# Performance work log

Measured on AMD Instinct MI355X. Metric: run time of the kernel, lower is better.

Reference implementation:

```python
import jax, jax.numpy as jnp
import numpy as np

N, E, R, D, P = 40000, 640000, 500, 128, 3

def setup_inputs() -> dict:
    key = jax.random.key(0)
    ks = jax.random.split(key, 14)
    return {
        "h": jax.random.normal(ks[0], (N, D), jnp.float32),
        "pos_enc": jax.random.normal(ks[1], (N, P), jnp.float32),
        "norm": jax.random.uniform(ks[2], (N, 1), jnp.float32),
        "emb_rel": jax.random.normal(ks[3], (R, D), jnp.float32),
        "W_hp": jax.random.normal(ks[4], (D + P, D), jnp.float32) / np.sqrt(D + P),
        "b_hp": jax.random.normal(ks[5], (D,), jnp.float32) * 0.01,
        "weight_neighbor": jax.random.normal(ks[6], (D, D), jnp.float32) / np.sqrt(D),
        "loop_weight": jax.random.normal(ks[7], (D, D), jnp.float32) / np.sqrt(D),
        "evolve_loop_weight": jax.random.normal(ks[8], (D, D), jnp.float32) / np.sqrt(D),
        "loop_weight_p": jax.random.normal(ks[9], (P, P), jnp.float32),
        "evolve_loop_weight_p": jax.random.normal(ks[10], (P, P), jnp.float32),
        "edge_src": jax.random.randint(ks[11], (E,), 0, N),
        "edge_dst": jax.random.randint(ks[12], (E,), 0, N),
        "edge_type": jax.random.randint(ks[13], (E,), 0, R),
    }

def reference(h, pos_enc, norm, emb_rel, W_hp, b_hp, weight_neighbor,
              loop_weight, evolve_loop_weight, loop_weight_p, evolve_loop_weight_p,
              edge_src, edge_dst, edge_type):
    n = h.shape[0]
    # self-loop: nodes with in-degree > 0 use loop_weight, else evolve_loop_weight
    in_deg = jax.ops.segment_sum(jnp.ones_like(edge_dst, dtype=h.dtype), edge_dst, num_segments=n)
    has_in = (in_deg > 0)[:, None]
    loop_msg = jnp.where(has_in, h @ loop_weight, h @ evolve_loop_weight)
    loop_msg_p = jnp.where(has_in, pos_enc @ loop_weight_p, pos_enc @ evolve_loop_weight_p)
    # per-edge message: embedding_hp(cat(h_src, pos_src)) + rel_emb[type], then weight_neighbor
    src_feat = jnp.concatenate([h[edge_src], pos_enc[edge_src]], axis=1)  # [E, D+P]
    e_h = src_feat @ W_hp + b_hp                                          # [E, D]
    msg = (e_h + emb_rel[edge_type]) @ weight_neighbor                    # [E, D]
    # scatter-sum to destination nodes, then norm scaling (apply_func)
    agg = jax.ops.segment_sum(msg, edge_dst, num_segments=n) * norm       # [N, D]
    node_repr = jax.nn.relu(agg + loop_msg)
    pos_out = jax.nn.relu(pos_enc + loop_msg_p)
    return node_repr, pos_out
```

## Files before the change

### kernel.cpp

```cpp
#include <hip/hip_runtime.h>


#define BS 1536
#define CAP2 48
#define CH 8192

typedef __bf16 bf16x8 __attribute__((ext_vector_type(8)));
typedef float f32x4 __attribute__((ext_vector_type(4)));
typedef unsigned short u16x4 __attribute__((ext_vector_type(4)));

__device__ inline unsigned short f2bf(float f) {
    unsigned u = __float_as_uint(f);
    u += 0x7fffu + ((u >> 16) & 1u);
    return (unsigned short)(u >> 16);
}
__device__ inline float bflo(unsigned u) { return __uint_as_float(u << 16); }
__device__ inline float bfhi(unsigned u) { return __uint_as_float(u & 0xffff0000u); }

__global__ __launch_bounds__(256) void k_pack(const float* __restrict__ Whp,
                                              int* __restrict__ gcnt,
                                              unsigned short* __restrict__ Whpfrag,
                                              int nbkt) {
    const int gid = blockIdx.x * blockDim.x + threadIdx.x;
    const int gs = gridDim.x * blockDim.x;
    for (int i = gid; i < nbkt; i += gs) gcnt[i] = 0;
    for (int i = gid; i < 16384; i += gs) {
        int j = i & 7, l = (i >> 3) & 63, nt = (i >> 9) & 7, c = i >> 12;
        int k = c * 32 + ((l >> 4) << 3) + j;
        int n = nt * 16 + (l & 15);
        Whpfrag[i] = f2bf(Whp[k * 128 + n]);
    }
}

__global__ __launch_bounds__(512) void k_comb(const float* __restrict__ h,
                                              const float* __restrict__ pos,
                                              const float* __restrict__ Whp,
                                              const unsigned short* __restrict__ Whpfrag,
                                              unsigned short* __restrict__ t,
                                              const int* __restrict__ esrc,
                                              const int* __restrict__ edst,
                                              const int* __restrict__ etyp, int E,
                                              int* __restrict__ gcnt,
                                              unsigned* __restrict__ gbuf,
                                              const float* __restrict__ emb, int embN,
                                              const float* __restrict__ Wn,
                                              const float* __restrict__ Lw,
                                              const float* __restrict__ Ew,
                                              unsigned short* __restrict__ emb16,
                                              unsigned short* __restrict__ Wfrag,
                                              int nBB, int nPB,
                                              int nbkt, int N) {
    __shared__ unsigned short hsh[64][136];
    __shared__ float WpS[3][128];
    __shared__ float posS[64][4];
    const int tid = threadIdx.x;

    if (blockIdx.x < nBB) {
        int* lcnt = reinterpret_cast<int*>(&hsh[0][0]);
        int* lbase = lcnt + 1280;
        const int e0 = blockIdx.x * CH;
        const int eN = min(E - e0, CH);
        for (int i = tid; i < nbkt; i += 512) lcnt[i] = 0;
        __syncthreads();
        for (int base = tid * 4; base < eN; base += 2048) {
            if (base + 3 < eN) {
                int4 d4 = *reinterpret_cast<const int4*>(&edst[e0 + base]);
                atomicAdd(&lcnt[d4.x >> 5], 1);
                atomicAdd(&lcnt[d4.y >> 5], 1);
                atomicAdd(&lcnt[d4.z >> 5], 1);
                atomicAdd(&lcnt[d4.w >> 5], 1);
            } else {
                for (int k = 0; k < 4 && base + k < eN; k++)
                    atomicAdd(&lcnt[edst[e0 + base + k] >> 5], 1);
            }
        }
        __syncthreads();
        for (int i = tid; i < nbkt; i += 512) {
            int c = lcnt[i];
            lbase[i] = c ? atomicAdd(&gcnt[i], c) : 0;
        }
        __syncthreads();
        for (int i = tid; i < nbkt; i += 512) lcnt[i] = 0;
        __syncthreads();
        for (int base = tid * 4; base < eN; base += 2048) {
            if (base + 3 < eN) {
                int4 d4 = *reinterpret_cast<const int4*>(&edst[e0 + base]);
                int4 s4 = *reinterpret_cast<const int4*>(&esrc[e0 + base]);
                int4 t4 = *reinterpret_cast<const int4*>(&etyp[e0 + base]);
                int dd[4] = {d4.x, d4.y, d4.z, d4.w};
                int ss[4] = {s4.x, s4.y, s4.z, s4.w};
                int tt[4] = {t4.x, t4.y, t4.z, t4.w};
#pragma unroll
                for (int k = 0; k < 4; k++) {
                    int b = dd[k] >> 5;
                    unsigned val = (unsigned)(dd[k] & 31) | ((unsigned)ss[k] << 5)
                                 | ((unsigned)tt[k] << 21);
                    int off = atomicAdd(&lcnt[b], 1);
                    gbuf[(size_t)b * BS + min(lbase[b] + off, BS - 1)] = val;
                }
            } else {
                for (int k = 0; k < 4 && base + k < eN; k++) {
                    int d = edst[e0 + base + k];
                    int b = d >> 5;
                    unsigned val = (unsigned)(d & 31) | ((unsigned)esrc[e0 + base + k] << 5)
                                 | ((unsigned)etyp[e0 + base + k] << 21);
                    int off = atomicAdd(&lcnt[b], 1);
                    gbuf[(size_t)b * BS + min(lbase[b] + off, BS - 1)] = val;
                }
            }
        }
        return;
    }

    if (blockIdx.x < nBB + nPB) {
        const int base = (blockIdx.x - nBB) * 512 + tid;
        const int gs = nPB * 512;
        for (int i = base; i < 49152; i += gs) {
            int j = i & 7, l = (i >> 3) & 63, nt = (i >> 9) & 7, c = i >> 12;
            int k = c * 32 + ((l >> 4) << 3) + j;
            int n = nt * 16 + (l & 15);
            float v = (k < 128) ? Wn[k * 128 + n]
                    : (k < 256) ? Lw[(k - 128) * 128 + n]
                                : Ew[(k - 256) * 128 + n];
            Wfrag[i] = f2bf(v);
        }
        for (int i = base; i < embN; i += gs) emb16[i] = f2bf(emb[i]);
        return;
    }

    const int rbase = (blockIdx.x - nBB - nPB) * 64;
    const int w = tid >> 6, l = tid & 63;
    for (int i = tid; i < 384; i += 512) WpS[i >> 7][i & 127] = Whp[128 * 128 + i];
    if (tid < 192) {
        int r = tid / 3, j = tid % 3;
        int row = rbase + r;
        posS[r][j] = (row < N) ? pos[(size_t)row * 3 + j] : 0.f;
    }
#pragma unroll
    for (int it = 0; it < 4; it++) {
        int qid = tid + it * 512;
        int rr = qid >> 5, cq = qid & 31;
        int row = rbase + rr;
        u16x4 v = {0, 0, 0, 0};
        if (row < N) {
            float4 a = *reinterpret_cast<const float4*>(h + (size_t)row * 128 + cq * 4);
            v[0] = f2bf(a.x); v[1] = f2bf(a.y); v[2] = f2bf(a.z); v[3] = f2bf(a.w);
        }
        *reinterpret_cast<u16x4*>(&hsh[rr][cq * 4]) = v;
    }
    __syncthreads();

    f32x4 acc[4];
#pragma unroll
    for (int i = 0; i < 4; i++) acc[i] = (f32x4){0.f, 0.f, 0.f, 0.f};
    const int rt = w >> 1, ch = w & 1;
#pragma unroll
    for (int c = 0; c < 4; c++) {
        bf16x8 a = *reinterpret_cast<const bf16x8*>(&hsh[rt * 16 + (l & 15)][c * 32 + (l >> 4) * 8]);
        const bf16x8* Bp = reinterpret_cast<const bf16x8*>(Whpfrag) + (size_t)c * 512;
#pragma unroll
        for (int n2 = 0; n2 < 4; n2++) {
            bf16x8 b = Bp[(ch * 4 + n2) * 64 + l];
            acc[n2] = __builtin_amdgcn_mfma_f32_16x16x32_bf16(a, b, acc[n2], 0, 0, 0);
        }
    }
    const int lrow0 = rt * 16 + ((l >> 4) << 2);
#pragma unroll
    for (int n2 = 0; n2 < 4; n2++) {
        int col = (ch * 4 + n2) * 16 + (l & 15);
        float w0 = WpS[0][col], w1 = WpS[1][col], w2 = WpS[2][col];
#pragma unroll
        for (int r = 0; r < 4; r++) {
            int lr = lrow0 + r;
            int grow = rbase + lr;
            if (grow < N) {
                float v = acc[n2][r] + posS[lr][0] * w0 + posS[lr][1] * w1 + posS[lr][2] * w2;
                t[(size_t)grow * 128 + col] = f2bf(v);
            }
        }
    }
}

__global__ __launch_bounds__(512) void k_fused(const float* __restrict__ h,
                                               const float* __restrict__ pos,
                                               const float* __restrict__ nrm,
                                               const float* __restrict__ bhp,
                                               const unsigned short* __restrict__ t,
                                               const unsigned short* __restrict__ emb16,
                                               const int* __restrict__ gcnt,
                                               const unsigned* __restrict__ gbuf,
                                               const unsigned short* __restrict__ Wfrag,
                                               const float* __restrict__ Lwp,
                                               const float* __restrict__ Ewp,
                                               float* __restrict__ out, int N) {
    __shared__ unsigned eplists[32][CAP2];
    __shared__ int lcnt2[32];
    __shared__ unsigned short x0sh[32][136];
    __shared__ unsigned short hsh[32][136];
    __shared__ float bsh[128];
    __shared__ float nrmS[32];
    const int tid = threadIdx.x;
    const int rbase = blockIdx.x * 32;
    const int w = tid >> 6, lane = tid & 63;
    const int half = lane >> 5;
    const int g = (lane >> 4) & 1, l16 = lane & 15;

    if (tid < 128) bsh[tid] = bhp[tid];
    if (tid < 32) {
        int row = rbase + tid;
        nrmS[tid] = (row < N) ? nrm[row] : 0.f;
        lcnt2[tid] = 0;
    }
    __syncthreads();

    const int cntB = min(gcnt[blockIdx.x], BS);
    for (int i = tid; i < cntB; i += 512) {
        unsigned v = gbuf[(size_t)blockIdx.x * BS + i];
        int d = v & 31;
        int off = atomicAdd(&lcnt2[d], 1);
        if (off < CAP2) eplists[d][off] = v >> 5;
    }
    __syncthreads();

    const uint4* tw4 = reinterpret_cast<const uint4*>(t);
    const uint4* ew4 = reinterpret_cast<const uint4*>(emb16);

#pragma unroll 1
    for (int p = 0; p < 2; p++) {
        const int base2 = p * 16 + w * 2;
        const int vl = base2 + half;
        const int m = min(lcnt2[vl], CAP2);
        const int mm = max(min(lcnt2[base2], CAP2), min(lcnt2[base2 + 1], CAP2));
        float a[8];
#pragma unroll
        for (int r = 0; r < 8; r++) a[r] = 0.f;
        const unsigned* epr = &eplists[vl][0];
#pragma unroll 1
        for (int j = 0; j < mm; j += 8) {
            uint4 tv[4], ev[4];
            float sel[4];
#pragma unroll
            for (int u = 0; u < 4; u++) {
                int idx = j + 2 * u + g;
                unsigned pe = epr[min(idx, CAP2 - 1)];
                bool val = idx < m;
                unsigned pk = val ? pe : 0u;
                sel[u] = val ? 1.f : 0.f;
                tv[u] = tw4[(pk & 0xffffu) * 16u + l16];
                ev[u] = ew4[(pk >> 16) * 16u + l16];
            }
#pragma unroll
            for (int u = 0; u < 4; u++) {
                a[0] = fmaf(sel[u], bflo(tv[u].x) + bflo(ev[u].x), a[0]);
                a[1] = fmaf(sel[u], bfhi(tv[u].x) + bfhi(ev[u].x), a[1]);
                a[2] = fmaf(sel[u], bflo(tv[u].y) + bflo(ev[u].y), a[2]);
                a[3] = fmaf(sel[u], bfhi(tv[u].y) + bfhi(ev[u].y), a[3]);
                a[4] = fmaf(sel[u], bflo(tv[u].z) + bflo(ev[u].z), a[4]);
                a[5] = fmaf(sel[u], bfhi(tv[u].z) + bfhi(ev[u].z), a[5]);
                a[6] = fmaf(sel[u], bflo(tv[u].w) + bflo(ev[u].w), a[6]);
                a[7] = fmaf(sel[u], bfhi(tv[u].w) + bfhi(ev[u].w), a[7]);
            }
        }
#pragma unroll
        for (int r = 0; r < 8; r++) a[r] += __shfl_xor(a[r], 16);
        if (g == 0) {
            float dg = (float)lcnt2[vl], nf = nrmS[vl];
            unsigned pk4[4];
#pragma unroll
            for (int q = 0; q < 4; q++) {
                float lo = nf * (a[2 * q]     + dg * bsh[l16 * 8 + 2 * q]);
                float hi = nf * (a[2 * q + 1] + dg * bsh[l16 * 8 + 2 * q + 1]);
                pk4[q] = (unsigned)f2bf(lo) | ((unsigned)f2bf(hi) << 16);
            }
            *reinterpret_cast<uint4*>(&x0sh[vl][l16 * 8]) =
                make_uint4(pk4[0], pk4[1], pk4[2], pk4[3]);
        }
    }

#pragma unroll
    for (int it = 0; it < 2; it++) {
        int qid = tid + it * 512;
        int rr = qid >> 5, cq = qid & 31;
        int row = rbase + rr;
        float4 a = make_float4(0.f, 0.f, 0.f, 0.f);
        if (row < N)
            a = *reinterpret_cast<const float4*>(h + (size_t)row * 128 + cq * 4);
        u16x4 vv;
        vv[0] = f2bf(a.x); vv[1] = f2bf(a.y);
        vv[2] = f2bf(a.z); vv[3] = f2bf(a.w);
        *reinterpret_cast<u16x4*>(&hsh[rr][cq * 4]) = vv;
    }
    __syncthreads();

    f32x4 acc[2];
    acc[0] = (f32x4){0.f, 0.f, 0.f, 0.f};
    acc[1] = (f32x4){0.f, 0.f, 0.f, 0.f};
    const int rt = w >> 2, ch = w & 3;
    const int arow = rt * 16 + (lane & 15);
    const bool fl = (lcnt2[arow] > 0);
#pragma unroll
    for (int c = 0; c < 12; c++) {
        uint4 raw;
        if (c < 4) {
            raw = *reinterpret_cast<const uint4*>(&x0sh[arow][c * 32 + (lane >> 4) * 8]);
        } else {
            raw = *reinterpret_cast<const uint4*>(&hsh[arow][(c & 3) * 32 + (lane >> 4) * 8]);
            bool keep = (c < 8) ? fl : !fl;
            if (!keep) { raw.x = 0; raw.y = 0; raw.z = 0; raw.w = 0; }
        }
        bf16x8 a = *reinterpret_cast<bf16x8*>(&raw);
        const bf16x8* Bp = reinterpret_cast<const bf16x8*>(Wfrag) + (size_t)c * 512;
#pragma unroll
        for (int n2 = 0; n2 < 2; n2++) {
            bf16x8 b = Bp[(ch * 2 + n2) * 64 + lane];
            acc[n2] = __builtin_amdgcn_mfma_f32_16x16x32_bf16(a, b, acc[n2], 0, 0, 0);
        }
    }
    const int lrow0 = rt * 16 + ((lane >> 4) << 2);
#pragma unroll
    for (int n2 = 0; n2 < 2; n2++) {
        int col = (ch * 2 + n2) * 16 + (lane & 15);
#pragma unroll
        for (int r = 0; r < 4; r++) {
            int grow = rbase + lrow0 + r;
            if (grow < N)
                out[(size_t)grow * 128 + col] = fmaxf(acc[n2][r], 0.f);
        }
    }
    if (tid < 32) {
        int row = rbase + tid;
        if (row < N) {
            float p0 = pos[(size_t)row * 3 + 0];
            float p1 = pos[(size_t)row * 3 + 1];
            float p2 = pos[(size_t)row * 3 + 2];
            const float* M = (lcnt2[tid] > 0) ? Lwp : Ewp;
            float o0 = p0 + (p0 * M[0] + p1 * M[3] + p2 * M[6]);
            float o1 = p1 + (p0 * M[1] + p1 * M[4] + p2 * M[7]);
            float o2 = p2 + (p0 * M[2] + p1 * M[5] + p2 * M[8]);
            size_t base = (size_t)N * 128 + (size_t)row * 3;
            out[base + 0] = fmaxf(o0, 0.f);
            out[base + 1] = fmaxf(o1, 0.f);
            out[base + 2] = fmaxf(o2, 0.f);
        }
    }
}

extern "C" void kernel_launch(void* const* d_in, const int* in_sizes, int n_in,
                              void* d_out, int out_size, void* d_ws, size_t ws_size,
                              hipStream_t stream) {
    const float* h   = (const float*)d_in[0];
    const float* pos = (const float*)d_in[1];
    const float* nrm = (const float*)d_in[2];
    const float* emb = (const float*)d_in[3];
    const float* Whp = (const float*)d_in[4];
    const float* bhp = (const float*)d_in[5];
    const float* Wn  = (const float*)d_in[6];
    const float* Lw  = (const float*)d_in[7];
    const float* Ew  = (const float*)d_in[8];
    const float* Lwp = (const float*)d_in[9];
    const float* Ewp = (const float*)d_in[10];
    const int* esrc  = (const int*)d_in[11];
    const int* edst  = (const int*)d_in[12];
    const int* etyp  = (const int*)d_in[13];

    const int N = in_sizes[2];
    const int E = in_sizes[11];
    const int embN = in_sizes[3];

    float* out = (float*)d_out;

    char* wsb = (char*)d_ws;
    size_t off = 0;
    auto nalloc = [&](size_t bytes) { char* p = wsb + off; off += (bytes + 255) & ~(size_t)255; return p; };
    const int nbkt = (N + 31) / 32;
    unsigned short* t       = (unsigned short*)nalloc((size_t)N * 128 * 2);
    int*            gcnt    = (int*)nalloc((size_t)nbkt * 4);
    unsigned*       gbuf    = (unsigned*)nalloc((size_t)nbkt * BS * 4);
    unsigned short* emb16   = (unsigned short*)nalloc((size_t)embN * 2);
    unsigned short* Wfrag   = (unsigned short*)nalloc(49152 * 2);
    unsigned short* Whpfrag = (unsigned short*)nalloc(16384 * 2);

    k_pack<<<64, 256, 0, stream>>>(Whp, gcnt, Whpfrag, nbkt);
    const int nTB = (N + 63) / 64;
    const int nBB = (E + CH - 1) / CH;
    const int nPB = 32;
    k_comb<<<nBB + nPB + nTB, 512, 0, stream>>>(h, pos, Whp, Whpfrag, t,
                                                esrc, edst, etyp, E,
                                                gcnt, gbuf,
                                                emb, embN, Wn, Lw, Ew,
                                                emb16, Wfrag, nBB, nPB, nbkt, N);
    k_fused<<<nbkt, 512, 0, stream>>>(h, pos, nrm, bhp, t, emb16, gcnt, gbuf,
                                      Wfrag, Lwp, Ewp, out, N);
}
```

Measured before the change: 67.42 us.

## Drop evolve-weight MFMA chunk, add rare-row fallback, reuse bf16 copy of h

The final GEMM in k_fused now multiplies only the Wn and Lw chunks, cutting its K dimension from 12 to 8 chunks. Rows with zero in-degree, which previously selected Ew through masking, are listed in shared memory and recomputed with a scalar fp32 dot product against Ew. k_comb also writes a bf16 copy of h while it is already converting h, so k_fused loads h16 instead of re-reading and re-converting fp32 h. The trade-off is an extra 10MB global write in k_comb and a slow serial path that only pays off when zero-degree rows are rare.

New measurement: 64.95 us. 3.7% less time.

```diff
diff --git a/kernel.cpp b/kernel.cpp
--- a/kernel.cpp
+++ b/kernel.cpp
@@ -37,6 +37,7 @@
                                               const float* __restrict__ Whp,
                                               const unsigned short* __restrict__ Whpfrag,
                                               unsigned short* __restrict__ t,
+                                              unsigned short* __restrict__ h16,
                                               const int* __restrict__ esrc,
                                               const int* __restrict__ edst,
                                               const int* __restrict__ etyp, int E,
@@ -45,7 +46,6 @@
                                               const float* __restrict__ emb, int embN,
                                               const float* __restrict__ Wn,
                                               const float* __restrict__ Lw,
-                                              const float* __restrict__ Ew,
                                               unsigned short* __restrict__ emb16,
                                               unsigned short* __restrict__ Wfrag,
                                               int nBB, int nPB,
@@ -115,13 +115,11 @@
     if (blockIdx.x < nBB + nPB) {
         const int base = (blockIdx.x - nBB) * 512 + tid;
         const int gs = nPB * 512;
-        for (int i = base; i < 49152; i += gs) {
+        for (int i = base; i < 32768; i += gs) {
             int j = i & 7, l = (i >> 3) & 63, nt = (i >> 9) & 7, c = i >> 12;
             int k = c * 32 + ((l >> 4) << 3) + j;
             int n = nt * 16 + (l & 15);
-            float v = (k < 128) ? Wn[k * 128 + n]
-                    : (k < 256) ? Lw[(k - 128) * 128 + n]
-                                : Ew[(k - 256) * 128 + n];
+            float v = (k < 128) ? Wn[k * 128 + n] : Lw[(k - 128) * 128 + n];
             Wfrag[i] = f2bf(v);
         }
         for (int i = base; i < embN; i += gs) emb16[i] = f2bf(emb[i]);
@@ -145,6 +143,7 @@
         if (row < N) {
             float4 a = *reinterpret_cast<const float4*>(h + (size_t)row * 128 + cq * 4);
             v[0] = f2bf(a.x); v[1] = f2bf(a.y); v[2] = f2bf(a.z); v[3] = f2bf(a.w);
+            *reinterpret_cast<u16x4*>(&h16[(size_t)row * 128 + cq * 4]) = v;
         }
         *reinterpret_cast<u16x4*>(&hsh[rr][cq * 4]) = v;
     }
@@ -186,10 +185,12 @@
                                                const float* __restrict__ nrm,
                                                const float* __restrict__ bhp,
                                                const unsigned short* __restrict__ t,
+                                               const unsigned short* __restrict__ h16,
                                                const unsigned short* __restrict__ emb16,
                                                const int* __restrict__ gcnt,
                                                const unsigned* __restrict__ gbuf,
                                                const unsigned short* __restrict__ Wfrag,
+                                               const float* __restrict__ Ew,
                                                const float* __restrict__ Lwp,
                                                const float* __restrict__ Ewp,
                                                float* __restrict__ out, int N) {
@@ -199,6 +200,8 @@
     __shared__ unsigned short hsh[32][136];
     __shared__ float bsh[128];
     __shared__ float nrmS[32];
+    __shared__ int zrowsS[32];
+    __shared__ int nzS;
     const int tid = threadIdx.x;
     const int rbase = blockIdx.x * 32;
     const int w = tid >> 6, lane = tid & 63;
@@ -206,6 +209,7 @@
     const int g = (lane >> 4) & 1, l16 = lane & 15;
 
     if (tid < 128) bsh[tid] = bhp[tid];
+    if (tid == 128) nzS = 0;
     if (tid < 32) {
         int row = rbase + tid;
         nrmS[tid] = (row < N) ? nrm[row] : 0.f;
@@ -221,6 +225,14 @@
         if (off < CAP2) eplists[d][off] = v >> 5;
     }
     __syncthreads();
+
+    if (tid < 32) {
+        int row = rbase + tid;
+        if (row < N && lcnt2[tid] == 0) {
+            int o = atomicAdd(&nzS, 1);
+            zrowsS[o] = tid;
+        }
+    }
 
     const uint4* tw4 = reinterpret_cast<const uint4*>(t);
     const uint4* ew4 = reinterpret_cast<const uint4*>(emb16);
@@ -277,18 +289,13 @@
         }
     }
 
-#pragma unroll
-    for (int it = 0; it < 2; it++) {
-        int qid = tid + it * 512;
-        int rr = qid >> 5, cq = qid & 31;
+    {
+        int rr = tid >> 4, q = tid & 15;
         int row = rbase + rr;
-        float4 a = make_float4(0.f, 0.f, 0.f, 0.f);
+        uint4 v = make_uint4(0, 0, 0, 0);
         if (row < N)
-            a = *reinterpret_cast<const float4*>(h + (size_t)row * 128 + cq * 4);
-        u16x4 vv;
-        vv[0] = f2bf(a.x); vv[1] = f2bf(a.y);
-        vv[2] = f2bf(a.z); vv[3] = f2bf(a.w);
-        *reinterpret_cast<u16x4*>(&hsh[rr][cq * 4]) = vv;
+            v = reinterpret_cast<const uint4*>(h16)[(size_t)row * 16 + q];
+        *reinterpret_cast<uint4*>(&hsh[rr][q * 8]) = v;
     }
     __syncthreads();
 
@@ -297,17 +304,13 @@
     acc[1] = (f32x4){0.f, 0.f, 0.f, 0.f};
     const int rt = w >> 2, ch = w & 3;
     const int arow = rt * 16 + (lane & 15);
-    const bool fl = (lcnt2[arow] > 0);
-#pragma unroll
-    for (int c = 0; c < 12; c++) {
+#pragma unroll
+    for (int c = 0; c < 8; c++) {
         uint4 raw;
-        if (c < 4) {
+        if (c < 4)
             raw = *reinterpret_cast<const uint4*>(&x0sh[arow][c * 32 + (lane >> 4) * 8]);
-        } else {
+        else
             raw = *reinterpret_cast<const uint4*>(&hsh[arow][(c & 3) * 32 + (lane >> 4) * 8]);
-            bool keep = (c < 8) ? fl : !fl;
-            if (!keep) { raw.x = 0; raw.y = 0; raw.z = 0; raw.w = 0; }
-        }
         bf16x8 a = *reinterpret_cast<bf16x8*>(&raw);
         const bf16x8* Bp = reinterpret_cast<const bf16x8*>(Wfrag) + (size_t)c * 512;
 #pragma unroll
@@ -322,9 +325,20 @@
         int col = (ch * 2 + n2) * 16 + (lane & 15);
 #pragma unroll
         for (int r = 0; r < 4; r++) {
-            int grow = rbase + lrow0 + r;
-            if (grow < N)
+            int lr = lrow0 + r;
+            int grow = rbase + lr;
+            if (grow < N && lcnt2[lr] > 0)
                 out[(size_t)grow * 128 + col] = fmaxf(acc[n2][r], 0.f);
+        }
+    }
+    for (int zi = 0; zi < nzS; zi++) {
+        int r = zrowsS[zi];
+        int row = rbase + r;
+        if (tid < 128) {
+            float accp = 0.f;
+            for (int k = 0; k < 128; k++)
+                accp += h[(size_t)row * 128 + k] * Ew[k * 128 + tid];
+            out[(size_t)row * 128 + tid] = fmaxf(accp, 0.f);
         }
     }
     if (tid < 32) {
@@ -374,21 +388,22 @@
     auto nalloc = [&](size_t bytes) { char* p = wsb + off; off += (bytes + 255) & ~(size_t)255; return p; };
     const int nbkt = (N + 31) / 32;
     unsigned short* t       = (unsigned short*)nalloc((size_t)N * 128 * 2);
+    unsigned short* h16     = (unsigned short*)nalloc((size_t)N * 128 * 2);
     int*            gcnt    = (int*)nalloc((size_t)nbkt * 4);
     unsigned*       gbuf    = (unsigned*)nalloc((size_t)nbkt * BS * 4);
     unsigned short* emb16   = (unsigned short*)nalloc((size_t)embN * 2);
-    unsigned short* Wfrag   = (unsigned short*)nalloc(49152 * 2);
+    unsigned short* Wfrag   = (unsigned short*)nalloc(32768 * 2);
     unsigned short* Whpfrag = (unsigned short*)nalloc(16384 * 2);
 
     k_pack<<<64, 256, 0, stream>>>(Whp, gcnt, Whpfrag, nbkt);
     const int nTB = (N + 63) / 64;
     const int nBB = (E + CH - 1) / CH;
     const int nPB = 32;
-    k_comb<<<nBB + nPB + nTB, 512, 0, stream>>>(h, pos, Whp, Whpfrag, t,
+    k_comb<<<nBB + nPB + nTB, 512, 0, stream>>>(h, pos, Whp, Whpfrag, t, h16,
                                                 esrc, edst, etyp, E,
                                                 gcnt, gbuf,
-                                                emb, embN, Wn, Lw, Ew,
+                                                emb, embN, Wn, Lw,
                                                 emb16, Wfrag, nBB, nPB, nbkt, N);
-    k_fused<<<nbkt, 512, 0, stream>>>(h, pos, nrm, bhp, t, emb16, gcnt, gbuf,
-                                      Wfrag, Lwp, Ewp, out, N);
+    k_fused<<<nbkt, 512, 0, stream>>>(h, pos, nrm, bhp, t, h16, emb16, gcnt, gbuf,
+                                      Wfrag, Ew, Lwp, Ewp, out, N);
 }
```
